# Kernel tuning notes

Hardware: AMD Instinct MI355X
Metric: run time of the kernel (lower is better)

The kernel has to match this reference:

```python
import jax, jax.numpy as jnp
import numpy as np
import math

B, A, S, H = 4, 3, 1024, 768
NH, HD = 12, 64  # num_heads, head_dim
TEMP = 1.0
LN_EPS = 1e-5


def setup_inputs() -> dict:
    key = jax.random.key(0)
    ks = jax.random.split(key, 8)
    w_scale = math.sqrt(6.0 / (H + H))  # xavier_uniform
    def lin_w(k):
        return jax.random.uniform(k, (H, H), jnp.float32, -w_scale, w_scale)
    return {
        "query": jax.random.normal(ks[0], (B, S, H), jnp.float32),
        "adapter_outputs": jax.random.normal(ks[1], (B, A, S, H), jnp.float32),
        "Wq": lin_w(ks[2]), "bq": jnp.zeros((H,), jnp.float32),
        "Wk": lin_w(ks[3]), "bk": jnp.zeros((H,), jnp.float32),
        "Wv": lin_w(ks[4]), "bv": jnp.zeros((H,), jnp.float32),
        "Wo": lin_w(ks[5]), "bo": jnp.zeros((H,), jnp.float32),
        "gamma": jnp.ones((H,), jnp.float32),
        "beta": jnp.zeros((H,), jnp.float32),
    }


def reference(query, adapter_outputs, Wq, bq, Wk, bk, Wv, bv, Wo, bo, gamma, beta):
    # Q: [B,S,H] -> [B,NH,S,HD]
    Q = (query @ Wq.T + bq).reshape(B, S, NH, HD).transpose(0, 2, 1, 3)
    # K,V: [B,A,S,H] -> [B,NH,A,S,HD] (vectorizes the per-adapter torch loop)
    K = (adapter_outputs @ Wk.T + bk).reshape(B, A, S, NH, HD).transpose(0, 3, 1, 2, 4)
    V = (adapter_outputs @ Wv.T + bv).reshape(B, A, S, NH, HD).transpose(0, 3, 1, 2, 4)
    scores = jnp.einsum('bhqd,bhasd->bhqas', Q, K) / (math.sqrt(HD) * TEMP)
    # softmax over the ADAPTER axis only (dim=3), as in the original
    attn = jax.nn.softmax(scores, axis=3)
    # sum over both adapters and source positions
    attended = jnp.einsum('bhqas,bhasd->bhqd', attn, V)
    attended = attended.transpose(0, 2, 1, 3).reshape(B, S, H)
    out = attended @ Wo.T + bo
    x = out + query
    mu = jnp.mean(x, axis=-1, keepdims=True)
    var = jnp.mean(jnp.square(x - mu), axis=-1, keepdims=True)
    out = (x - mu) * jax.lax.rsqrt(var + LN_EPS) * gamma + beta
    avg_weights = attn.mean(axis=1).mean(axis=2)  # [B,Q,S]
    return out, avg_weights
```

## Files before the change

kernel.cpp:

```cpp
#include <hip/hip_runtime.h>

#define NB 4
#define NA 3
#define NS 1024
#define NHID 768
#define NHEADS 12
#define HD 64

typedef __bf16 bf16_t;
typedef __bf16 bf16x8 __attribute__((ext_vector_type(8)));
typedef __bf16 bf16x4 __attribute__((ext_vector_type(4)));
typedef float f32x4 __attribute__((ext_vector_type(4)));

#define MFMA(a, b, c) __builtin_amdgcn_mfma_f32_16x16x32_bf16(a, b, c, 0, 0, 0)

static __device__ __forceinline__ bf16x8 load8(const bf16_t* p) {
    return *reinterpret_cast<const bf16x8*>(p);
}

typedef __attribute__((address_space(3))) unsigned int u32_lds;
typedef __attribute__((address_space(1))) unsigned int u32_glb;
static __device__ __forceinline__ void gl_lds16(const void* g, void* lds_base_uniform) {
    __builtin_amdgcn_global_load_lds((const u32_glb*)g, (u32_lds*)lds_base_uniform, 16, 0, 0);
}

static __device__ __forceinline__ bf16x8 cvt8(f32x4 lo, f32x4 hi) {
    bf16x8 r;
    r[0] = (bf16_t)lo[0]; r[1] = (bf16_t)lo[1]; r[2] = (bf16_t)lo[2]; r[3] = (bf16_t)lo[3];
    r[4] = (bf16_t)hi[0]; r[5] = (bf16_t)hi[1]; r[6] = (bf16_t)hi[2]; r[7] = (bf16_t)hi[3];
    return r;
}

__global__ __launch_bounds__(256) void cvt6(
    const float* __restrict__ s0, bf16_t* __restrict__ d0, int c0,
    const float* __restrict__ s1, bf16_t* __restrict__ d1, int c1,
    const float* __restrict__ s2, bf16_t* __restrict__ d2, int c2,
    const float* __restrict__ s3, bf16_t* __restrict__ d3, int c3,
    const float* __restrict__ s4, bf16_t* __restrict__ d4, int c4,
    const float* __restrict__ s5, bf16_t* __restrict__ d5, int c5)
{
    const int bid = blockIdx.x;
    const float* s; bf16_t* d; int rel;
    if      (bid < c0) { s = s0; d = d0; rel = bid; }
    else if (bid < c1) { s = s1; d = d1; rel = bid - c0; }
    else if (bid < c2) { s = s2; d = d2; rel = bid - c1; }
    else if (bid < c3) { s = s3; d = d3; rel = bid - c2; }
    else if (bid < c4) { s = s4; d = d4; rel = bid - c3; }
    else               { s = s5; d = d5; rel = bid - c4; }
    const int t = threadIdx.x;
#pragma unroll
    for (int k = 0; k < 4; k++) {
        size_t u = (size_t)rel * 1024 + k * 256 + t;
        f32x4 v = reinterpret_cast<const f32x4*>(s)[u];
        bf16x4 o;
        o[0] = (bf16_t)v[0]; o[1] = (bf16_t)v[1];
        o[2] = (bf16_t)v[2]; o[3] = (bf16_t)v[3];
        reinterpret_cast<bf16x4*>(d)[u] = o;
    }
}

template <int MODE, int NT, bool ABF, bool BBF>
__global__ __launch_bounds__(256) void proj_gemm(
    const void* __restrict__ Xv,
    const void* __restrict__ W0v, const void* __restrict__ W1v,
    const float* __restrict__ bias0, const float* __restrict__ bias1,
    const float* __restrict__ resid,
    bf16_t* __restrict__ out0, bf16_t* __restrict__ out1,
    float* __restrict__ outf,
    const void* __restrict__ X2, const void* __restrict__ W2v,
    const float* __restrict__ bias2, bf16_t* __restrict__ out2)
{
    constexpr int ASZ   = ABF ? 8192 : 16384;
    constexpr int BSZ   = BBF ? 8192 : 16384;
    constexpr int BUFSZ = ASZ + BSZ;
    constexpr int LPS   = (ABF ? 2 : 4) + (BBF ? 2 : 4);
    __shared__ __align__(16) char smem[3 * BUFSZ];

    const int t = threadIdx.x;
    const int lane = t & 63, w = t >> 6;
    const int quad = lane >> 4, l15 = lane & 15;
    const int wm = w >> 1, wn = w & 1;

    int emode = (MODE == 4) ? 1 : MODE;
    int nt    = NT;
    int bid   = blockIdx.x;
    const void*  Xp  = Xv;
    const void*  W0p = W0v;
    const float* b0  = bias0;
    bf16_t*      o0  = out0;
    if constexpr (MODE == 4) {
        if (bid >= 1152) {
            emode = 0; nt = 6; bid -= 1152;
            Xp = X2; W0p = W2v; b0 = bias2; o0 = out2;
        }
    }

    const int xcd = bid & 7, jj = bid >> 3;
    const int n_t = jj % nt, slab = jj / nt;
    const int m0 = (slab * 8 + xcd) * 128;
    const int n0 = n_t * 128;

    const void* Wselv = (emode == 1 && n0 >= 768) ? W1v : W0p;
    const int n0b = (emode == 1 && n0 >= 768) ? n0 - 768 : n0;

    const int srow  = lane >> 3;
    const int schnk = (lane & 7) ^ srow;
    const float*  Apf[4];
    const bf16_t* Apb[2];
    const float*  Bpf[4];
    const bf16_t* Bpb[2];
    if constexpr (ABF) {
        const bf16_t* X = (const bf16_t*)Xp;
#pragma unroll
        for (int i = 0; i < 2; i++) {
            int g = w * 2 + i;
            Apb[i] = X + (size_t)(m0 + g * 16 + l15) * NHID + quad * 8;
        }
    } else {
        const float* X = (const float*)Xp;
#pragma unroll
        for (int i = 0; i < 4; i++) {
            int g = w * 4 + i;
            Apf[i] = X + (size_t)(m0 + g * 8 + srow) * NHID + schnk * 4;
        }
    }
    if constexpr (BBF) {
        const bf16_t* Wb = (const bf16_t*)Wselv;
#pragma unroll
        for (int i = 0; i < 2; i++) {
            int g = w * 2 + i;
            Bpb[i] = Wb + (size_t)(n0b + g * 16 + l15) * NHID + quad * 8;
        }
    } else {
        const float* Wf = (const float*)Wselv;
#pragma unroll
        for (int i = 0; i < 4; i++) {
            int g = w * 4 + i;
            Bpf[i] = Wf + (size_t)(n0b + g * 8 + srow) * NHID + schnk * 4;
        }
    }

    auto stage = [&](char* base) {
        char* Ab = base;
        char* Bb = base + ASZ;
        if constexpr (ABF) {
#pragma unroll
            for (int i = 0; i < 2; i++) {
                gl_lds16(Apb[i], Ab + (w * 2 + i) * 1024);
                Apb[i] += 32;
            }
        } else {
#pragma unroll
            for (int i = 0; i < 4; i++) {
                gl_lds16(Apf[i], Ab + (w * 4 + i) * 1024);
                Apf[i] += 32;
            }
        }
        if constexpr (BBF) {
#pragma unroll
            for (int i = 0; i < 2; i++) {
                gl_lds16(Bpb[i], Bb + (w * 2 + i) * 1024);
                Bpb[i] += 32;
            }
        } else {
#pragma unroll
            for (int i = 0; i < 4; i++) {
                gl_lds16(Bpf[i], Bb + (w * 4 + i) * 1024);
                Bpf[i] += 32;
            }
        }
    };

    auto wait_one = [&]() {
        if constexpr (LPS == 4)      asm volatile("s_waitcnt vmcnt(4)" ::: "memory");
        else if constexpr (LPS == 6) asm volatile("s_waitcnt vmcnt(6)" ::: "memory");
        else                         asm volatile("s_waitcnt vmcnt(8)" ::: "memory");
    };

    f32x4 acc[4][4];
#pragma unroll
    for (int i = 0; i < 4; i++)
#pragma unroll
        for (int j = 0; j < 4; j++) acc[i][j] = 0.0f;

    constexpr int KITER = NHID / 32;
    stage(smem);
    stage(smem + BUFSZ);
    int put = 2, get = 0;

    for (int it = 0; it < KITER; ++it) {
        if (it == KITER - 1) asm volatile("s_waitcnt vmcnt(0)" ::: "memory");
        else                 wait_one();
        __builtin_amdgcn_s_barrier();
        if (it + 2 < KITER) {
            stage(smem + put * BUFSZ);
            put = (put == 2) ? 0 : put + 1;
        }

        char* Ab = smem + get * BUFSZ;
        char* Bb = Ab + ASZ;
        get = (get == 2) ? 0 : get + 1;

        bf16x8 af[4], bfr[4];
        const int pl = (2 * quad) ^ (l15 & 7);
#pragma unroll
        for (int i = 0; i < 4; i++) {
            if constexpr (ABF) {
                int mt = wm * 4 + i;
                af[i] = *(const bf16x8*)(Ab + (mt * 64 + lane) * 16);
            } else {
                int R = (wm * 4 + i) * 16 + l15;
                f32x4 lo = *(const f32x4*)(Ab + R * 128 + pl * 16);
                f32x4 hi = *(const f32x4*)(Ab + R * 128 + (pl ^ 1) * 16);
                af[i] = cvt8(lo, hi);
            }
        }
#pragma unroll
        for (int j = 0; j < 4; j++) {
            if constexpr (BBF) {
                int ntj = wn * 4 + j;
                bfr[j] = *(const bf16x8*)(Bb + (ntj * 64 + lane) * 16);
            } else {
                int R = (wn * 4 + j) * 16 + l15;
                f32x4 lo = *(const f32x4*)(Bb + R * 128 + pl * 16);
                f32x4 hi = *(const f32x4*)(Bb + R * 128 + (pl ^ 1) * 16);
                bfr[j] = cvt8(lo, hi);
            }
        }
#pragma unroll
        for (int i = 0; i < 4; i++)
#pragma unroll
            for (int j = 0; j < 4; j++)
                acc[i][j] = MFMA(af[i], bfr[j], acc[i][j]);
    }

#pragma unroll
    for (int i = 0; i < 4; i++) {
#pragma unroll
        for (int j = 0; j < 4; j++) {
            const int n = n0 + wn * 64 + j * 16 + l15;
            float bn;
            if (emode == 1) bn = (n < 768) ? b0[n] : bias1[n - 768];
            else            bn = b0[n];
#pragma unroll
            for (int rg = 0; rg < 4; rg++) {
                const int m = m0 + wm * 64 + i * 16 + quad * 4 + rg;
                float v = acc[i][j][rg] + bn;
                if (emode == 0) {
                    int b = m >> 10, s = m & 1023, hh = n >> 6, d = n & 63;
                    o0[(((size_t)(b * NHEADS + hh) * NS) + s) * HD + d] = (bf16_t)v;
                } else if (emode == 1) {
                    int b = m / (NA * NS);
                    int rem = m - b * (NA * NS);
                    int a = rem >> 10, s = rem & 1023;
                    if (n < 768) {
                        int hh = n >> 6, d = n & 63;
                        o0[((((size_t)(b * NHEADS + hh) * NA + a) * NS) + s) * HD + d] = (bf16_t)v;
                    } else {
                        int hh = (n - 768) >> 6, d = (n - 768) & 63;
                        int sp = (s & ~31) | (quad << 3) | ((i & 1) << 2) | rg;
                        out1[((((size_t)(b * NHEADS + hh) * NA + a) * HD) + d) * NS + sp] = (bf16_t)v;
                    }
                } else {
                    v += resid[(size_t)m * NHID + n];
                    outf[(size_t)m * NHID + n] = v;
                }
            }
        }
    }
}

__global__ __launch_bounds__(256, 3) void attn_kernel(
    const bf16_t* __restrict__ Q, const bf16_t* __restrict__ K,
    const bf16_t* __restrict__ VT, bf16_t* __restrict__ AT)
{
    __shared__ __align__(16) char kv[2 * 24576];

    const int t    = threadIdx.x;
    const int w    = t >> 6, lane = t & 63;
    const int quad = lane >> 4, l15 = lane & 15;

    int bh, qt;
    if (gridDim.x == 768) {
        int xcd = blockIdx.x & 7, j = blockIdx.x >> 3;
        bh = (j >> 4) * 8 + xcd;
        qt = ((j & 15) << 2) | w;
    } else {
        bh = blockIdx.x >> 4;
        qt = ((blockIdx.x & 15) << 2) | w;
    }
    const int b  = bh / NHEADS, h = bh - b * NHEADS;
    const int q0 = qt * 16;

    const bf16_t* Qb = Q + ((size_t)bh * NS + q0) * HD;
    bf16x8 qf0 = load8(Qb + l15 * HD + quad * 8);
    bf16x8 qf1 = load8(Qb + l15 * HD + quad * 8 + 32);

    const char* gp[6];
    int gdelta[6], loff[6];
#pragma unroll
    for (int i = 0; i < 6; i++) {
        int g = w * 6 + i;
        loff[i] = g >= 12 ? 12288 + (g - 12) * 1024 : g * 1024;
        if (g < 12) {
            int a = g >> 2, j = (g >> 1) & 1, dh = g & 1;
            gp[i] = (const char*)(K + ((size_t)(bh * NA + a) * NS + j * 16 + l15) * HD
                                  + dh * 32 + quad * 8);
            gdelta[i] = 32 * HD * 2;
        } else {
            int gi = g - 12;
            int a = gi >> 2, dt = gi & 3;
            gp[i] = (const char*)(VT + ((size_t)(bh * NA + a) * HD + dt * 16 + l15) * NS
                                  + quad * 8);
            gdelta[i] = 32 * 2;
        }
    }

    auto stage = [&](int buf) {
#pragma unroll
        for (int i = 0; i < 6; i++) {
            gl_lds16(gp[i], kv + buf * 24576 + loff[i]);
            gp[i] += gdelta[i];
        }
    };

    f32x4 acc[4];
#pragma unroll
    for (int dt = 0; dt < 4; dt++) acc[dt] = 0.0f;

    const float KS = 0.18033688011112042f;

    stage(0);
    __syncthreads();

    for (int it = 0; it < 32; ++it) {
        if (it + 1 < 32) stage((it + 1) & 1);

        const char* base = kv + (it & 1) * 24576;
        f32x4 sc[3][2];
#pragma unroll
        for (int a = 0; a < 3; a++) {
#pragma unroll
            for (int j = 0; j < 2; j++) {
                bf16x8 klo = *(const bf16x8*)(base + ((a * 4 + j * 2 + 0) * 64 + lane) * 16);
                bf16x8 khi = *(const bf16x8*)(base + ((a * 4 + j * 2 + 1) * 64 + lane) * 16);
                f32x4 z = 0.0f;
                f32x4 c0 = MFMA(klo, qf0, z);
                sc[a][j] = MFMA(khi, qf1, c0);
            }
        }
        f32x4 plo[3], phi[3];
#pragma unroll
        for (int j = 0; j < 2; j++) {
#pragma unroll
            for (int rg = 0; rg < 4; rg++) {
                float x0 = sc[0][j][rg], x1 = sc[1][j][rg], x2 = sc[2][j][rg];
                float mx = fmaxf(x0, fmaxf(x1, x2));
                float e0 = __builtin_amdgcn_exp2f((x0 - mx) * KS);
                float e1 = __builtin_amdgcn_exp2f((x1 - mx) * KS);
                float e2 = __builtin_amdgcn_exp2f((x2 - mx) * KS);
                float inv = __builtin_amdgcn_rcpf(e0 + e1 + e2);
                if (j == 0) {
                    plo[0][rg] = e0 * inv; plo[1][rg] = e1 * inv; plo[2][rg] = e2 * inv;
                } else {
                    phi[0][rg] = e0 * inv; phi[1][rg] = e1 * inv; phi[2][rg] = e2 * inv;
                }
            }
        }
#pragma unroll
        for (int a = 0; a < 3; a++) {
            bf16x8 pf = cvt8(plo[a], phi[a]);
#pragma unroll
            for (int dt = 0; dt < 4; dt++) {
                bf16x8 vf = *(const bf16x8*)(base + 12288 + ((a * 4 + dt) * 64 + lane) * 16);
                acc[dt] = MFMA(pf, vf, acc[dt]);
            }
        }
        __syncthreads();
    }

    bf16_t* Ob = AT + (size_t)b * NS * NHID;
#pragma unroll
    for (int dt = 0; dt < 4; dt++) {
#pragma unroll
        for (int rg = 0; rg < 4; rg++) {
            int qq = q0 + quad * 4 + rg;
            Ob[(size_t)qq * NHID + h * HD + dt * 16 + l15] = (bf16_t)acc[dt][rg];
        }
    }
}

__global__ __launch_bounds__(256) void ln_kernel(
    float* __restrict__ X, const float* __restrict__ gamma,
    const float* __restrict__ beta)
{
    const int row = blockIdx.x;
    const int t = threadIdx.x;
    float* x = X + (size_t)row * NHID;
    float v0 = x[t], v1 = x[t + 256], v2 = x[t + 512];
    float s  = v0 + v1 + v2;
    float s2 = v0 * v0 + v1 * v1 + v2 * v2;
#pragma unroll
    for (int off = 32; off > 0; off >>= 1) {
        s  += __shfl_down(s, off);
        s2 += __shfl_down(s2, off);
    }
    __shared__ float red[8];
    const int w = t >> 6, lane = t & 63;
    if (lane == 0) { red[w] = s; red[4 + w] = s2; }
    __syncthreads();
    s  = red[0] + red[1] + red[2] + red[3];
    s2 = red[4] + red[5] + red[6] + red[7];
    float mu  = s * (1.0f / NHID);
    float var = s2 * (1.0f / NHID) - mu * mu;
    float rs  = rsqrtf(fmaxf(var, 0.0f) + 1e-5f);
    x[t]       = (v0 - mu) * rs * gamma[t]       + beta[t];
    x[t + 256] = (v1 - mu) * rs * gamma[t + 256] + beta[t + 256];
    x[t + 512] = (v2 - mu) * rs * gamma[t + 512] + beta[t + 512];
}

__global__ __launch_bounds__(256) void fill_third(float* __restrict__ p)
{
    const int i = blockIdx.x * 256 + threadIdx.x;
    f32x4 v = { 1.0f / 3.0f, 1.0f / 3.0f, 1.0f / 3.0f, 1.0f / 3.0f };
    *reinterpret_cast<f32x4*>(p + (size_t)i * 4) = v;
}

extern "C" void kernel_launch(void* const* d_in, const int* in_sizes, int n_in,
                              void* d_out, int out_size, void* d_ws, size_t ws_size,
                              hipStream_t stream)
{
    (void)in_sizes; (void)n_in; (void)out_size;
    const float* query = (const float*)d_in[0];
    const float* adapt = (const float*)d_in[1];
    const float* Wq    = (const float*)d_in[2];
    const float* bq    = (const float*)d_in[3];
    const float* Wk    = (const float*)d_in[4];
    const float* bk    = (const float*)d_in[5];
    const float* Wv    = (const float*)d_in[6];
    const float* bv    = (const float*)d_in[7];
    const float* Wo    = (const float*)d_in[8];
    const float* bo    = (const float*)d_in[9];
    const float* gamma = (const float*)d_in[10];
    const float* beta  = (const float*)d_in[11];

    float*  out0  = (float*)d_out;
    float*  out1f = out0 + 3145728;
    bf16_t* out1b = (bf16_t*)out1f;

    dim3 blk(256);

    if (ws_size >= (size_t)67633152) {
        bf16_t* Kw  = (bf16_t*)d_ws;
        bf16_t* VTw = (bf16_t*)((char*)d_ws + 18874368);
        bf16_t* Adb = (bf16_t*)((char*)d_ws + 37748736);
        bf16_t* Wqb = (bf16_t*)((char*)d_ws + 56623104);
        bf16_t* Wkb = (bf16_t*)((char*)d_ws + 57802752);
        bf16_t* Wvb = (bf16_t*)((char*)d_ws + 58982400);
        bf16_t* Wob = (bf16_t*)((char*)d_ws + 60162048);
        bf16_t* Qcb = (bf16_t*)((char*)d_ws + 61341696);
        bf16_t* Qw  = out1b;
        bf16_t* ATw = out1b + 3145728;
        cvt6<<<dim3(3648), blk, 0, stream>>>(
            adapt, Adb, 2304, query, Qcb, 3072,
            Wq, Wqb, 3216, Wk, Wkb, 3360, Wv, Wvb, 3504, Wo, Wob, 3648);
        proj_gemm<4, 12, true, true><<<dim3(1344), blk, 0, stream>>>(
            Adb, Wkb, Wvb, bk, bv, nullptr, Kw, VTw, nullptr,
            Qcb, Wqb, bq, Qw);
        attn_kernel<<<dim3(768), blk, 0, stream>>>(Qw, Kw, VTw, ATw);
        proj_gemm<3, 6, true, true><<<dim3(192), blk, 0, stream>>>(
            ATw, Wob, nullptr, bo, nullptr, query, nullptr, nullptr, out0,
            nullptr, nullptr, nullptr, nullptr);
    } else if (ws_size >= (size_t)37748736) {
        bf16_t* Kw  = (bf16_t*)d_ws;
        bf16_t* VTw = (bf16_t*)((char*)d_ws + 18874368);
        bf16_t* Qw  = out1b;
        bf16_t* ATw = out1b + 3145728;
        bf16_t* Wqb = out1b + 6291456;
        bf16_t* Wkb = Wqb + 589824;
        bf16_t* Wvb = Wkb + 589824;
        cvt6<<<dim3(432), blk, 0, stream>>>(
            Wq, Wqb, 144, Wk, Wkb, 288, Wv, Wvb, 432,
            Wv, Wvb, 432, Wv, Wvb, 432, Wv, Wvb, 432);
        proj_gemm<0, 6, false, true><<<dim3(192), blk, 0, stream>>>(
            query, Wqb, nullptr, bq, nullptr, nullptr, Qw, nullptr, nullptr,
            nullptr, nullptr, nullptr, nullptr);
        proj_gemm<1, 12, false, true><<<dim3(1152), blk, 0, stream>>>(
            adapt, Wkb, Wvb, bk, bv, nullptr, Kw, VTw, nullptr,
            nullptr, nullptr, nullptr, nullptr);
        attn_kernel<<<dim3(768), blk, 0, stream>>>(Qw, Kw, VTw, ATw);
        proj_gemm<3, 6, true, false><<<dim3(192), blk, 0, stream>>>(
            ATw, Wo, nullptr, bo, nullptr, query, nullptr, nullptr, out0,
            nullptr, nullptr, nullptr, nullptr);
    } else {
        bf16_t* Qc  = out1b;
        bf16_t* ATc = out1b + 786432;
        bf16_t* Kc  = out1b + 1572864;
        bf16_t* VTc = out1b + 3932160;
        for (int b = 0; b < NB; b++) {
            const float* qb = query + (size_t)b * NS * NHID;
            const float* ab = adapt + (size_t)b * NA * NS * NHID;
            proj_gemm<0, 6, false, false><<<dim3(48), blk, 0, stream>>>(
                qb, Wq, nullptr, bq, nullptr, nullptr, Qc, nullptr, nullptr,
                nullptr, nullptr, nullptr, nullptr);
            proj_gemm<1, 12, false, false><<<dim3(288), blk, 0, stream>>>(
                ab, Wk, Wv, bk, bv, nullptr, Kc, VTc, nullptr,
                nullptr, nullptr, nullptr, nullptr);
            attn_kernel<<<dim3(192), blk, 0, stream>>>(Qc, Kc, VTc, ATc);
            proj_gemm<3, 6, true, false><<<dim3(48), blk, 0, stream>>>(
                ATc, Wo, nullptr, bo, nullptr, qb, nullptr, nullptr,
                out0 + (size_t)b * NS * NHID,
                nullptr, nullptr, nullptr, nullptr);
        }
    }

    ln_kernel<<<dim3(4096), blk, 0, stream>>>(out0, gamma, beta);
    fill_third<<<dim3(4096), blk, 0, stream>>>(out1f);
}
```

Measured before the change: 315.0 us.

## Add single-wave 64x64 GEMM and MFMA-fragment-tiled V layout for attention loads

Introduces a new one-wave-per-block 64x64-tile GEMM (wgemm) used for the fused K/V/Q projection and the output projection in the large-workspace path, replacing the 256-thread 128x128 proj_gemm there. V is now stored in a pre-swizzled MFMA-fragment-tiled layout written via LDS staging with coalesced 16-byte stores. The attention kernel loads V as contiguous per-lane 16-byte chunks instead of strided transposed rows. This aims at better occupancy, more blocks and cheaper V writes and loads, at the cost of less data reuse per block and more global traffic for A and B tiles.

```diff
diff --git a/kernel.cpp b/kernel.cpp
--- a/kernel.cpp
+++ b/kernel.cpp
@@ -30,6 +30,7 @@
     r[4] = (bf16_t)hi[0]; r[5] = (bf16_t)hi[1]; r[6] = (bf16_t)hi[2]; r[7] = (bf16_t)hi[3];
     return r;
 }
+
 
 __global__ __launch_bounds__(256) void cvt6(
     const float* __restrict__ s0, bf16_t* __restrict__ d0, int c0,
@@ -59,6 +60,142 @@
     }
 }
 
+template <int WMODE, int NT>
+__global__ __launch_bounds__(64) void wgemm(
+    const bf16_t* __restrict__ X,
+    const bf16_t* __restrict__ W0, const bf16_t* __restrict__ W1,
+    const float* __restrict__ bias0, const float* __restrict__ bias1,
+    const float* __restrict__ resid,
+    bf16_t* __restrict__ out0, bf16_t* __restrict__ outV,
+    float* __restrict__ outf,
+    const bf16_t* __restrict__ X2, const bf16_t* __restrict__ W2,
+    const float* __restrict__ bias2, bf16_t* __restrict__ out2)
+{
+    __shared__ __align__(16) char smem[2][8192];
+
+    const int lane = threadIdx.x & 63;
+    const int quad = lane >> 4, l15 = lane & 15;
+
+    int emode = (WMODE == 4) ? 1 : WMODE;
+    int nt    = NT;
+    int bid   = blockIdx.x;
+    const bf16_t* Xp = X;
+    const bf16_t* Wp = W0;
+    const float*  b0 = bias0;
+    bf16_t*       o0 = out0;
+    if constexpr (WMODE == 4) {
+        if (bid >= 4608) {
+            emode = 0; nt = 12; bid -= 4608;
+            Xp = X2; Wp = W2; b0 = bias2; o0 = out2;
+        }
+    }
+    const int xcd = bid & 7, jj = bid >> 3;
+    const int n_t = jj % nt, slab = jj / nt;
+    const int m0 = (slab * 8 + xcd) * 64;
+    const int n0 = n_t * 64;
+
+    const bf16_t* Wsel = (emode == 1 && n0 >= 768) ? W1 : Wp;
+    const int n0b = (emode == 1 && n0 >= 768) ? n0 - 768 : n0;
+
+    const bf16_t* Ap[4];
+    const bf16_t* Bp[4];
+#pragma unroll
+    for (int i = 0; i < 4; i++) {
+        Ap[i] = Xp   + (size_t)(m0  + i * 16 + l15) * NHID + quad * 8;
+        Bp[i] = Wsel + (size_t)(n0b + i * 16 + l15) * NHID + quad * 8;
+    }
+    auto stage = [&](char* base) {
+#pragma unroll
+        for (int i = 0; i < 4; i++) { gl_lds16(Ap[i], base + i * 1024);        Ap[i] += 32; }
+#pragma unroll
+        for (int i = 0; i < 4; i++) { gl_lds16(Bp[i], base + 4096 + i * 1024); Bp[i] += 32; }
+    };
+
+    f32x4 acc[4][4];
+#pragma unroll
+    for (int i = 0; i < 4; i++)
+#pragma unroll
+        for (int j = 0; j < 4; j++) acc[i][j] = 0.0f;
+
+    constexpr int KITER = NHID / 32;
+    stage(smem[0]);
+    stage(smem[1]);
+
+    for (int it = 0; it < KITER; ++it) {
+        if (it == KITER - 1) asm volatile("s_waitcnt vmcnt(0)" ::: "memory");
+        else                 asm volatile("s_waitcnt vmcnt(8)" ::: "memory");
+        char* cur = smem[it & 1];
+        bf16x8 af[4], bfr[4];
+#pragma unroll
+        for (int i = 0; i < 4; i++) af[i]  = *(const bf16x8*)(cur + (i * 64 + lane) * 16);
+#pragma unroll
+        for (int j = 0; j < 4; j++) bfr[j] = *(const bf16x8*)(cur + 4096 + (j * 64 + lane) * 16);
+        asm volatile("s_waitcnt lgkmcnt(0)" ::: "memory");
+        if (it + 2 < KITER) stage(cur);
+#pragma unroll
+        for (int i = 0; i < 4; i++)
+#pragma unroll
+            for (int j = 0; j < 4; j++)
+                acc[i][j] = MFMA(af[i], bfr[j], acc[i][j]);
+    }
+
+    if (emode == 1 && n0 >= 768) {
+        char* img = smem[0];
+        const int hh  = (n0 - 768) >> 6;
+        const int b   = m0 / (NA * NS);
+        const int rem = m0 - b * (NA * NS);
+        const int a   = rem >> 10;
+        const int s0  = rem & 1023;
+#pragma unroll
+        for (int i = 0; i < 4; i++) {
+#pragma unroll
+            for (int j = 0; j < 4; j++) {
+                float bn = bias1[(n0 - 768) + j * 16 + l15];
+                bf16x4 pk;
+#pragma unroll
+                for (int rg = 0; rg < 4; rg++) pk[rg] = (bf16_t)(acc[i][j][rg] + bn);
+                int off = (i >> 1) * 4096 + j * 1024 + (quad * 16 + l15) * 16 + (i & 1) * 8;
+                *reinterpret_cast<bf16x4*>(img + off) = pk;
+            }
+        }
+        asm volatile("s_waitcnt lgkmcnt(0)" ::: "memory");
+        char* gbase = (char*)outV + (size_t)((b * NHEADS + hh) * NA + a) * 131072
+                      + (size_t)(s0 >> 5) * 4096;
+#pragma unroll
+        for (int p = 0; p < 8; p++) {
+            f32x4 v = *reinterpret_cast<const f32x4*>(img + p * 1024 + lane * 16);
+            *reinterpret_cast<f32x4*>(gbase + p * 1024 + lane * 16) = v;
+        }
+    } else {
+#pragma unroll
+        for (int i = 0; i < 4; i++) {
+#pragma unroll
+            for (int j = 0; j < 4; j++) {
+                const int n = n0 + j * 16 + l15;
+                const float bn = b0[n];
+#pragma unroll
+                for (int rg = 0; rg < 4; rg++) {
+                    const int m = m0 + i * 16 + quad * 4 + rg;
+                    float v = acc[i][j][rg] + bn;
+                    if (emode == 0) {
+                        int b = m >> 10, s = m & 1023, hh = n >> 6, d = n & 63;
+                        o0[(((size_t)(b * NHEADS + hh) * NS) + s) * HD + d] = (bf16_t)v;
+                    } else if (emode == 1) {
+                        int b = m / (NA * NS);
+                        int rem = m - b * (NA * NS);
+                        int a = rem >> 10, s = rem & 1023;
+                        int hh = n >> 6, d = n & 63;
+                        o0[((((size_t)(b * NHEADS + hh) * NA + a) * NS) + s) * HD + d] = (bf16_t)v;
+                    } else {
+                        v += resid[(size_t)m * NHID + n];
+                        outf[(size_t)m * NHID + n] = v;
+                    }
+                }
+            }
+        }
+    }
+}
+
 template <int MODE, int NT, bool ABF, bool BBF>
 __global__ __launch_bounds__(256) void proj_gemm(
     const void* __restrict__ Xv,
@@ -66,9 +203,7 @@
     const float* __restrict__ bias0, const float* __restrict__ bias1,
     const float* __restrict__ resid,
     bf16_t* __restrict__ out0, bf16_t* __restrict__ out1,
-    float* __restrict__ outf,
-    const void* __restrict__ X2, const void* __restrict__ W2v,
-    const float* __restrict__ bias2, bf16_t* __restrict__ out2)
+    float* __restrict__ outf)
 {
     constexpr int ASZ   = ABF ? 8192 : 16384;
     constexpr int BSZ   = BBF ? 8192 : 16384;
@@ -81,27 +216,14 @@
     const int quad = lane >> 4, l15 = lane & 15;
     const int wm = w >> 1, wn = w & 1;
 
-    int emode = (MODE == 4) ? 1 : MODE;
-    int nt    = NT;
-    int bid   = blockIdx.x;
-    const void*  Xp  = Xv;
-    const void*  W0p = W0v;
-    const float* b0  = bias0;
-    bf16_t*      o0  = out0;
-    if constexpr (MODE == 4) {
-        if (bid >= 1152) {
-            emode = 0; nt = 6; bid -= 1152;
-            Xp = X2; W0p = W2v; b0 = bias2; o0 = out2;
-        }
-    }
-
+    const int bid = blockIdx.x;
     const int xcd = bid & 7, jj = bid >> 3;
-    const int n_t = jj % nt, slab = jj / nt;
+    const int n_t = jj % NT, slab = jj / NT;
     const int m0 = (slab * 8 + xcd) * 128;
     const int n0 = n_t * 128;
 
-    const void* Wselv = (emode == 1 && n0 >= 768) ? W1v : W0p;
-    const int n0b = (emode == 1 && n0 >= 768) ? n0 - 768 : n0;
+    const void* Wselv = (MODE == 1 && n0 >= 768) ? W1v : W0v;
+    const int n0b = (MODE == 1 && n0 >= 768) ? n0 - 768 : n0;
 
     const int srow  = lane >> 3;
     const int schnk = (lane & 7) ^ srow;
@@ -110,14 +232,14 @@
     const float*  Bpf[4];
     const bf16_t* Bpb[2];
     if constexpr (ABF) {
-        const bf16_t* X = (const bf16_t*)Xp;
+        const bf16_t* X = (const bf16_t*)Xv;
 #pragma unroll
         for (int i = 0; i < 2; i++) {
             int g = w * 2 + i;
             Apb[i] = X + (size_t)(m0 + g * 16 + l15) * NHID + quad * 8;
         }
     } else {
-        const float* X = (const float*)Xp;
+        const float* X = (const float*)Xv;
 #pragma unroll
         for (int i = 0; i < 4; i++) {
             int g = w * 4 + i;
@@ -145,29 +267,17 @@
         char* Bb = base + ASZ;
         if constexpr (ABF) {
 #pragma unroll
-            for (int i = 0; i < 2; i++) {
-                gl_lds16(Apb[i], Ab + (w * 2 + i) * 1024);
-                Apb[i] += 32;
-            }
+            for (int i = 0; i < 2; i++) { gl_lds16(Apb[i], Ab + (w * 2 + i) * 1024); Apb[i] += 32; }
         } else {
 #pragma unroll
-            for (int i = 0; i < 4; i++) {
-                gl_lds16(Apf[i], Ab + (w * 4 + i) * 1024);
-                Apf[i] += 32;
-            }
+            for (int i = 0; i < 4; i++) { gl_lds16(Apf[i], Ab + (w * 4 + i) * 1024); Apf[i] += 32; }
         }
         if constexpr (BBF) {
 #pragma unroll
-            for (int i = 0; i < 2; i++) {
-                gl_lds16(Bpb[i], Bb + (w * 2 + i) * 1024);
-                Bpb[i] += 32;
-            }
+            for (int i = 0; i < 2; i++) { gl_lds16(Bpb[i], Bb + (w * 2 + i) * 1024); Bpb[i] += 32; }
         } else {
 #pragma unroll
-            for (int i = 0; i < 4; i++) {
-                gl_lds16(Bpf[i], Bb + (w * 4 + i) * 1024);
-                Bpf[i] += 32;
-            }
+            for (int i = 0; i < 4; i++) { gl_lds16(Bpf[i], Bb + (w * 4 + i) * 1024); Bpf[i] += 32; }
         }
     };
 
@@ -240,30 +350,39 @@
         for (int j = 0; j < 4; j++) {
             const int n = n0 + wn * 64 + j * 16 + l15;
             float bn;
-            if (emode == 1) bn = (n < 768) ? b0[n] : bias1[n - 768];
-            else            bn = b0[n];
-#pragma unroll
-            for (int rg = 0; rg < 4; rg++) {
-                const int m = m0 + wm * 64 + i * 16 + quad * 4 + rg;
-                float v = acc[i][j][rg] + bn;
-                if (emode == 0) {
-                    int b = m >> 10, s = m & 1023, hh = n >> 6, d = n & 63;
-                    o0[(((size_t)(b * NHEADS + hh) * NS) + s) * HD + d] = (bf16_t)v;
-                } else if (emode == 1) {
-                    int b = m / (NA * NS);
-                    int rem = m - b * (NA * NS);
-                    int a = rem >> 10, s = rem & 1023;
-                    if (n < 768) {
+            if (MODE == 1) bn = (n < 768) ? bias0[n] : bias1[n - 768];
+            else           bn = bias0[n];
+            if (MODE == 1 && n >= 768) {
+                const int m = m0 + wm * 64 + i * 16 + quad * 4;
+                int b = m / (NA * NS);
+                int rem = m - b * (NA * NS);
+                int a = rem >> 10, s = rem & 1023;
+                int hh = (n - 768) >> 6;
+                bf16x4 pk;
+#pragma unroll
+                for (int rg = 0; rg < 4; rg++) pk[rg] = (bf16_t)(acc[i][j][rg] + bn);
+                char* dst = (char*)out1 + (size_t)((b * NHEADS + hh) * NA + a) * 131072
+                            + (size_t)(s >> 5) * 4096 + j * 1024
+                            + (quad * 16 + l15) * 16 + (i & 1) * 8;
+                *reinterpret_cast<bf16x4*>(dst) = pk;
+            } else {
+#pragma unroll
+                for (int rg = 0; rg < 4; rg++) {
+                    const int m = m0 + wm * 64 + i * 16 + quad * 4 + rg;
+                    float v = acc[i][j][rg] + bn;
+                    if (MODE == 0) {
+                        int b = m >> 10, s = m & 1023, hh = n >> 6, d = n & 63;
+                        out0[(((size_t)(b * NHEADS + hh) * NS) + s) * HD + d] = (bf16_t)v;
+                    } else if (MODE == 1) {
+                        int b = m / (NA * NS);
+                        int rem = m - b * (NA * NS);
+                        int a = rem >> 10, s = rem & 1023;
                         int hh = n >> 6, d = n & 63;
-                        o0[((((size_t)(b * NHEADS + hh) * NA + a) * NS) + s) * HD + d] = (bf16_t)v;
+                        out0[((((size_t)(b * NHEADS + hh) * NA + a) * NS) + s) * HD + d] = (bf16_t)v;
                     } else {
-                        int hh = (n - 768) >> 6, d = (n - 768) & 63;
-                        int sp = (s & ~31) | (quad << 3) | ((i & 1) << 2) | rg;
-                        out1[((((size_t)(b * NHEADS + hh) * NA + a) * HD) + d) * NS + sp] = (bf16_t)v;
+                        v += resid[(size_t)m * NHID + n];
+                        outf[(size_t)m * NHID + n] = v;
                     }
-                } else {
-                    v += resid[(size_t)m * NHID + n];
-                    outf[(size_t)m * NHID + n] = v;
                 }
             }
         }
@@ -310,9 +429,9 @@
         } else {
             int gi = g - 12;
             int a = gi >> 2, dt = gi & 3;
-            gp[i] = (const char*)(VT + ((size_t)(bh * NA + a) * HD + dt * 16 + l15) * NS
-                                  + quad * 8);
-            gdelta[i] = 32 * 2;
+            gp[i] = (const char*)VT + (size_t)(bh * NA + a) * 131072
+                    + dt * 1024 + (size_t)lane * 16;
+            gdelta[i] = 4096;
         }
     }
 
@@ -464,11 +583,11 @@
         cvt6<<<dim3(3648), blk, 0, stream>>>(
             adapt, Adb, 2304, query, Qcb, 3072,
             Wq, Wqb, 3216, Wk, Wkb, 3360, Wv, Wvb, 3504, Wo, Wob, 3648);
-        proj_gemm<4, 12, true, true><<<dim3(1344), blk, 0, stream>>>(
+        wgemm<4, 24><<<dim3(5376), dim3(64), 0, stream>>>(
             Adb, Wkb, Wvb, bk, bv, nullptr, Kw, VTw, nullptr,
             Qcb, Wqb, bq, Qw);
         attn_kernel<<<dim3(768), blk, 0, stream>>>(Qw, Kw, VTw, ATw);
-        proj_gemm<3, 6, true, true><<<dim3(192), blk, 0, stream>>>(
+        wgemm<3, 12><<<dim3(768), dim3(64), 0, stream>>>(
             ATw, Wob, nullptr, bo, nullptr, query, nullptr, nullptr, out0,
             nullptr, nullptr, nullptr, nullptr);
     } else if (ws_size >= (size_t)37748736) {
@@ -483,15 +602,12 @@
             Wq, Wqb, 144, Wk, Wkb, 288, Wv, Wvb, 432,
             Wv, Wvb, 432, Wv, Wvb, 432, Wv, Wvb, 432);
         proj_gemm<0, 6, false, true><<<dim3(192), blk, 0, stream>>>(
-            query, Wqb, nullptr, bq, nullptr, nullptr, Qw, nullptr, nullptr,
-            nullptr, nullptr, nullptr, nullptr);
+            query, Wqb, nullptr, bq, nullptr, nullptr, Qw, nullptr, nullptr);
         proj_gemm<1, 12, false, true><<<dim3(1152), blk, 0, stream>>>(
-            adapt, Wkb, Wvb, bk, bv, nullptr, Kw, VTw, nullptr,
-            nullptr, nullptr, nullptr, nullptr);
+            adapt, Wkb, Wvb, bk, bv, nullptr, Kw, VTw, nullptr);
         attn_kernel<<<dim3(768), blk, 0, stream>>>(Qw, Kw, VTw, ATw);
         proj_gemm<3, 6, true, false><<<dim3(192), blk, 0, stream>>>(
-            ATw, Wo, nullptr, bo, nullptr, query, nullptr, nullptr, out0,
-            nullptr, nullptr, nullptr, nullptr);
+            ATw, Wo, nullptr, bo, nullptr, query, nullptr, nullptr, out0);
     } else {
         bf16_t* Qc  = out1b;
         bf16_t* ATc = out1b + 786432;
@@ -501,16 +617,13 @@
             const float* qb = query + (size_t)b * NS * NHID;
             const float* ab = adapt + (size_t)b * NA * NS * NHID;
             proj_gemm<0, 6, false, false><<<dim3(48), blk, 0, stream>>>(
-                qb, Wq, nullptr, bq, nullptr, nullptr, Qc, nullptr, nullptr,
-                nullptr, nullptr, nullptr, nullptr);
+                qb, Wq, nullptr, bq, nullptr, nullptr, Qc, nullptr, nullptr);
             proj_gemm<1, 12, false, false><<<dim3(288), blk, 0, stream>>>(
-                ab, Wk, Wv, bk, bv, nullptr, Kc, VTc, nullptr,
-                nullptr, nullptr, nullptr, nullptr);
+                ab, Wk, Wv, bk, bv, nullptr, Kc, VTc, nullptr);
             attn_kernel<<<dim3(192), blk, 0, stream>>>(Qc, Kc, VTc, ATc);
             proj_gemm<3, 6, true, false><<<dim3(48), blk, 0, stream>>>(
                 ATc, Wo, nullptr, bo, nullptr, qb, nullptr, nullptr,
-                out0 + (size_t)b * NS * NHID,
-                nullptr, nullptr, nullptr, nullptr);
+                out0 + (size_t)b * NS * NHID);
         }
     }
 
```

After: 326.3 us. +3.6%, slower.

## Use double-buffered GEMM pipeline, pre-tiled V layout, and explicit vmcnt waits in attention

Applied to the files above, without the earlier changes.

The projection GEMM drops from a three-stage to a two-stage LDS ring. Each iteration now issues the next stage before waiting and adds a second barrier, which cuts LDS use and may let more blocks fit per CU. The V-projection epilogue writes 4-element packed stores straight into the tile layout the attention kernel stages, so attention reads V with contiguous 4KB strides instead of strided rows. Attention also swaps __syncthreads for explicit vmcnt waits plus raw barriers. The cost is less prefetch depth in the GEMM and one extra barrier per k-step.

```diff
diff --git a/kernel.cpp b/kernel.cpp
--- a/kernel.cpp
+++ b/kernel.cpp
@@ -30,6 +30,7 @@
     r[4] = (bf16_t)hi[0]; r[5] = (bf16_t)hi[1]; r[6] = (bf16_t)hi[2]; r[7] = (bf16_t)hi[3];
     return r;
 }
+
 
 __global__ __launch_bounds__(256) void cvt6(
     const float* __restrict__ s0, bf16_t* __restrict__ d0, int c0,
@@ -74,7 +75,7 @@
     constexpr int BSZ   = BBF ? 8192 : 16384;
     constexpr int BUFSZ = ASZ + BSZ;
     constexpr int LPS   = (ABF ? 2 : 4) + (BBF ? 2 : 4);
-    __shared__ __align__(16) char smem[3 * BUFSZ];
+    __shared__ __align__(16) char smem[2 * BUFSZ];
 
     const int t = threadIdx.x;
     const int lane = t & 63, w = t >> 6;
@@ -145,29 +146,17 @@
         char* Bb = base + ASZ;
         if constexpr (ABF) {
 #pragma unroll
-            for (int i = 0; i < 2; i++) {
-                gl_lds16(Apb[i], Ab + (w * 2 + i) * 1024);
-                Apb[i] += 32;
-            }
+            for (int i = 0; i < 2; i++) { gl_lds16(Apb[i], Ab + (w * 2 + i) * 1024); Apb[i] += 32; }
         } else {
 #pragma unroll
-            for (int i = 0; i < 4; i++) {
-                gl_lds16(Apf[i], Ab + (w * 4 + i) * 1024);
-                Apf[i] += 32;
-            }
+            for (int i = 0; i < 4; i++) { gl_lds16(Apf[i], Ab + (w * 4 + i) * 1024); Apf[i] += 32; }
         }
         if constexpr (BBF) {
 #pragma unroll
-            for (int i = 0; i < 2; i++) {
-                gl_lds16(Bpb[i], Bb + (w * 2 + i) * 1024);
-                Bpb[i] += 32;
-            }
+            for (int i = 0; i < 2; i++) { gl_lds16(Bpb[i], Bb + (w * 2 + i) * 1024); Bpb[i] += 32; }
         } else {
 #pragma unroll
-            for (int i = 0; i < 4; i++) {
-                gl_lds16(Bpf[i], Bb + (w * 4 + i) * 1024);
-                Bpf[i] += 32;
-            }
+            for (int i = 0; i < 4; i++) { gl_lds16(Bpf[i], Bb + (w * 4 + i) * 1024); Bpf[i] += 32; }
         }
     };
 
@@ -185,21 +174,18 @@
 
     constexpr int KITER = NHID / 32;
     stage(smem);
-    stage(smem + BUFSZ);
-    int put = 2, get = 0;
 
     for (int it = 0; it < KITER; ++it) {
-        if (it == KITER - 1) asm volatile("s_waitcnt vmcnt(0)" ::: "memory");
-        else                 wait_one();
+        if (it + 1 < KITER) {
+            stage(smem + ((it + 1) & 1) * BUFSZ);
+            wait_one();
+        } else {
+            asm volatile("s_waitcnt vmcnt(0)" ::: "memory");
+        }
         __builtin_amdgcn_s_barrier();
-        if (it + 2 < KITER) {
-            stage(smem + put * BUFSZ);
-            put = (put == 2) ? 0 : put + 1;
-        }
-
-        char* Ab = smem + get * BUFSZ;
+
+        char* Ab = smem + (it & 1) * BUFSZ;
         char* Bb = Ab + ASZ;
-        get = (get == 2) ? 0 : get + 1;
 
         bf16x8 af[4], bfr[4];
         const int pl = (2 * quad) ^ (l15 & 7);
@@ -232,6 +218,7 @@
 #pragma unroll
             for (int j = 0; j < 4; j++)
                 acc[i][j] = MFMA(af[i], bfr[j], acc[i][j]);
+        __builtin_amdgcn_s_barrier();
     }
 
 #pragma unroll
@@ -242,28 +229,37 @@
             float bn;
             if (emode == 1) bn = (n < 768) ? b0[n] : bias1[n - 768];
             else            bn = b0[n];
-#pragma unroll
-            for (int rg = 0; rg < 4; rg++) {
-                const int m = m0 + wm * 64 + i * 16 + quad * 4 + rg;
-                float v = acc[i][j][rg] + bn;
-                if (emode == 0) {
-                    int b = m >> 10, s = m & 1023, hh = n >> 6, d = n & 63;
-                    o0[(((size_t)(b * NHEADS + hh) * NS) + s) * HD + d] = (bf16_t)v;
-                } else if (emode == 1) {
-                    int b = m / (NA * NS);
-                    int rem = m - b * (NA * NS);
-                    int a = rem >> 10, s = rem & 1023;
-                    if (n < 768) {
+            if (emode == 1 && n >= 768) {
+                const int m = m0 + wm * 64 + i * 16 + quad * 4;
+                int b = m / (NA * NS);
+                int rem = m - b * (NA * NS);
+                int a = rem >> 10, s = rem & 1023;
+                int hh = (n - 768) >> 6;
+                bf16x4 pk;
+#pragma unroll
+                for (int rg = 0; rg < 4; rg++) pk[rg] = (bf16_t)(acc[i][j][rg] + bn);
+                char* dst = (char*)out1 + (size_t)((b * NHEADS + hh) * NA + a) * 131072
+                            + (size_t)(s >> 5) * 4096 + j * 1024
+                            + (quad * 16 + l15) * 16 + (i & 1) * 8;
+                *reinterpret_cast<bf16x4*>(dst) = pk;
+            } else {
+#pragma unroll
+                for (int rg = 0; rg < 4; rg++) {
+                    const int m = m0 + wm * 64 + i * 16 + quad * 4 + rg;
+                    float v = acc[i][j][rg] + bn;
+                    if (emode == 0) {
+                        int b = m >> 10, s = m & 1023, hh = n >> 6, d = n & 63;
+                        o0[(((size_t)(b * NHEADS + hh) * NS) + s) * HD + d] = (bf16_t)v;
+                    } else if (emode == 1) {
+                        int b = m / (NA * NS);
+                        int rem = m - b * (NA * NS);
+                        int a = rem >> 10, s = rem & 1023;
                         int hh = n >> 6, d = n & 63;
                         o0[((((size_t)(b * NHEADS + hh) * NA + a) * NS) + s) * HD + d] = (bf16_t)v;
                     } else {
-                        int hh = (n - 768) >> 6, d = (n - 768) & 63;
-                        int sp = (s & ~31) | (quad << 3) | ((i & 1) << 2) | rg;
-                        out1[((((size_t)(b * NHEADS + hh) * NA + a) * HD) + d) * NS + sp] = (bf16_t)v;
+                        v += resid[(size_t)m * NHID + n];
+                        outf[(size_t)m * NHID + n] = v;
                     }
-                } else {
-                    v += resid[(size_t)m * NHID + n];
-                    outf[(size_t)m * NHID + n] = v;
                 }
             }
         }
@@ -310,9 +306,9 @@
         } else {
             int gi = g - 12;
             int a = gi >> 2, dt = gi & 3;
-            gp[i] = (const char*)(VT + ((size_t)(bh * NA + a) * HD + dt * 16 + l15) * NS
-                                  + quad * 8);
-            gdelta[i] = 32 * 2;
+            gp[i] = (const char*)VT + (size_t)(bh * NA + a) * 131072
+                    + dt * 1024 + (size_t)lane * 16;
+            gdelta[i] = 4096;
         }
     }
 
@@ -331,10 +327,15 @@
     const float KS = 0.18033688011112042f;
 
     stage(0);
-    __syncthreads();
 
     for (int it = 0; it < 32; ++it) {
-        if (it + 1 < 32) stage((it + 1) & 1);
+        if (it + 1 < 32) {
+            stage((it + 1) & 1);
+            asm volatile("s_waitcnt vmcnt(6)" ::: "memory");
+        } else {
+            asm volatile("s_waitcnt vmcnt(0)" ::: "memory");
+        }
+        __builtin_amdgcn_s_barrier();
 
         const char* base = kv + (it & 1) * 24576;
         f32x4 sc[3][2];
@@ -376,7 +377,7 @@
                 acc[dt] = MFMA(pf, vf, acc[dt]);
             }
         }
-        __syncthreads();
+        __builtin_amdgcn_s_barrier();
     }
 
     bf16_t* Ob = AT + (size_t)b * NS * NHID;
```

Result: faster. 287.9 us (-8.6%).
